# Performance work log

Measured on AMD Instinct MI355X. Metric: run time of the kernel, lower is better.

Reference implementation:

```python
import jax, jax.numpy as jnp
import numpy as np

N = 100000   # nodes
E = 1600000  # edges (avg degree 16)
D = 128      # embedding / hidden dim
L = 2        # aggregator layers (len(weight_size_list)-1)
EPS = 1e-12  # F.normalize eps


def setup_inputs() -> dict:
    key = jax.random.key(0)
    ks = jax.random.split(key, 8)
    return {
        "embeddings": jax.random.normal(ks[0], (N, D), jnp.float32),
        "edge_src": jax.random.randint(ks[1], (E,), 0, N, jnp.int32),
        "edge_dst": jax.random.randint(ks[2], (E,), 0, N, jnp.int32),
        "edge_val": jax.random.uniform(ks[3], (E,), jnp.float32),
        "W_sum": jax.random.normal(ks[4], (L, D, D), jnp.float32) * 0.05,
        "b_sum": jnp.zeros((L, D), jnp.float32),
        "W_prod": jax.random.normal(ks[5], (L, D, D), jnp.float32) * 0.05,
        "b_prod": jnp.zeros((L, D), jnp.float32),
    }


def reference(embeddings, edge_src, edge_dst, edge_val, W_sum, b_sum, W_prod, b_prod):
    # Faithful KGATConv forward with BiAggregator (alg_type='bi'), dropout=0 (eval).
    # Note: original code feeds the UN-normalized aggregator output as `embeddings`
    # (ego) to the next layer, while the SpMM consumes the normalized all_embeddings[-1].
    ego = embeddings            # `embeddings` variable in torch code
    spmm_in = embeddings        # all_embeddings[-1]
    outs = [embeddings]
    for i in range(L):
        # sparse A @ x : gather source rows, scale by edge value, scatter-add to dst
        msg = edge_val[:, None] * spmm_in[edge_src]            # [E, D]
        side = jax.ops.segment_sum(msg, edge_dst, num_segments=N)  # [N, D]
        # BiAggregator: LeakyReLU(W1(e+side)+b1) + LeakyReLU(W2(e*side)+b2)
        s = jax.nn.leaky_relu((ego + side) @ W_sum[i] + b_sum[i], 0.01)
        p = jax.nn.leaky_relu((ego * side) @ W_prod[i] + b_prod[i], 0.01)
        ego = s + p
        # F.normalize(p=2, dim=-1)
        nrm = jnp.maximum(jnp.linalg.norm(ego, axis=-1, keepdims=True), EPS)
        spmm_in = ego / nrm
        outs.append(spmm_in)
    return jnp.stack(outs)  # [L+1, N, D]
```

## Files before the change

kernel.cpp:

```cpp
#include <hip/hip_runtime.h>

#define D_DIM 128
#define ROWS 32
#define MROWS 64
#define ZPAD 136
#define EPAD 132

#define BSH 7
#define BROWS (1 << BSH)
#define NB_MAX 2048
#define CHUNK 4096

typedef __bf16 bf16x8 __attribute__((ext_vector_type(8)));
typedef __bf16 bf16x4 __attribute__((ext_vector_type(4)));
typedef float  f32x4  __attribute__((ext_vector_type(4)));

__global__ __launch_bounds__(256) void spmm_atomic(
    const float* __restrict__ x, const int* __restrict__ src,
    const int* __restrict__ dst, const float* __restrict__ val,
    float* __restrict__ side, long long total)
{
    long long i = (long long)blockIdx.x * blockDim.x + threadIdx.x;
    if (i >= total) return;
    int e = (int)(i >> 5);
    int q = (int)(i & 31);
    int s = src[e];
    int d = dst[e];
    float v = val[e];
    const float4 xv = *reinterpret_cast<const float4*>(x + (long long)s * D_DIM + q * 4);
    float* o = side + (long long)d * D_DIM + q * 4;
    unsafeAtomicAdd(o + 0, v * xv.x);
    unsafeAtomicAdd(o + 1, v * xv.y);
    unsafeAtomicAdd(o + 2, v * xv.z);
    unsafeAtomicAdd(o + 3, v * xv.w);
}

__global__ __launch_bounds__(256) void hist_kernel(
    const int* __restrict__ dst, int* __restrict__ cnt, int E)
{
    int i = blockIdx.x * 256 + threadIdx.x;
    if (i < E) atomicAdd(&cnt[dst[i]], 1);
}

__global__ __launch_bounds__(256) void scan_blocks(
    const int* __restrict__ cnt, int* __restrict__ row_ptr,
    int* __restrict__ blk_sums, int N)
{
    __shared__ int sh[256];
    int i = blockIdx.x * 256 + threadIdx.x;
    int v = (i < N) ? cnt[i] : 0;
    sh[threadIdx.x] = v;
    __syncthreads();
#pragma unroll
    for (int off = 1; off < 256; off <<= 1) {
        int t = (threadIdx.x >= off) ? sh[threadIdx.x - off] : 0;
        __syncthreads();
        sh[threadIdx.x] += t;
        __syncthreads();
    }
    if (i < N) row_ptr[i] = sh[threadIdx.x] - v;
    if (threadIdx.x == 255) blk_sums[blockIdx.x] = sh[255];
}

__global__ __launch_bounds__(256) void scan_carry(int* __restrict__ blk, int B)
{
    __shared__ int sh[256];
    __shared__ int carry;
    if (threadIdx.x == 0) carry = 0;
    __syncthreads();
    for (int base = 0; base < B; base += 256) {
        int i = base + threadIdx.x;
        int v = (i < B) ? blk[i] : 0;
        sh[threadIdx.x] = v;
        __syncthreads();
#pragma unroll
        for (int off = 1; off < 256; off <<= 1) {
            int t = (threadIdx.x >= off) ? sh[threadIdx.x - off] : 0;
            __syncthreads();
            sh[threadIdx.x] += t;
            __syncthreads();
        }
        int excl = sh[threadIdx.x] - v + carry;
        if (i < B) blk[i] = excl;
        __syncthreads();
        if (threadIdx.x == 255) carry = carry + sh[255];
        __syncthreads();
    }
}

__global__ __launch_bounds__(256) void scan_add(
    int* __restrict__ row_ptr, const int* __restrict__ blk_sums,
    int* __restrict__ row_fill, int N, int E)
{
    int i = blockIdx.x * 256 + threadIdx.x;
    if (i < N) {
        int v = row_ptr[i] + blk_sums[i >> 8];
        row_ptr[i]  = v;
        row_fill[i] = v;
    }
    if (i == 0) row_ptr[N] = E;
}

__global__ __launch_bounds__(256) void scatter_kernel(
    const int* __restrict__ src, const int* __restrict__ dst,
    const float* __restrict__ val, int* __restrict__ row_fill,
    int2* __restrict__ csr_sv, int E)
{
    int e = blockIdx.x * 256 + threadIdx.x;
    if (e >= E) return;
    int d = dst[e];
    int pos = atomicAdd(&row_fill[d], 1);
    csr_sv[pos] = make_int2(src[e], __float_as_int(val[e]));
}

__global__ __launch_bounds__(256) void bucket_count(
    const int* __restrict__ dst, int* __restrict__ bucket_cnt, int E, int NB)
{
    __shared__ int h[NB_MAX];
    for (int i = threadIdx.x; i < NB; i += 256) h[i] = 0;
    __syncthreads();
    int ebase = blockIdx.x * CHUNK;
    int ecnt  = min(CHUNK, E - ebase);
    for (int i = threadIdx.x; i < ecnt; i += 256)
        atomicAdd(&h[dst[ebase + i] >> BSH], 1);
    __syncthreads();
    for (int i = threadIdx.x; i < NB; i += 256)
        if (h[i]) atomicAdd(&bucket_cnt[i], h[i]);
}

__global__ __launch_bounds__(256) void bucket_scan(
    const int* __restrict__ bucket_cnt, int* __restrict__ bucket_ptr,
    int* __restrict__ bucket_fill, int NB, int E)
{
    __shared__ int sh[256];
    __shared__ int carry;
    if (threadIdx.x == 0) carry = 0;
    __syncthreads();
    for (int base = 0; base < NB; base += 256) {
        int i = base + threadIdx.x;
        int v = (i < NB) ? bucket_cnt[i] : 0;
        sh[threadIdx.x] = v;
        __syncthreads();
#pragma unroll
        for (int off = 1; off < 256; off <<= 1) {
            int t = (threadIdx.x >= off) ? sh[threadIdx.x - off] : 0;
            __syncthreads();
            sh[threadIdx.x] += t;
            __syncthreads();
        }
        if (i < NB) {
            int excl = sh[threadIdx.x] - v + carry;
            bucket_ptr[i]  = excl;
            bucket_fill[i] = excl;
        }
        __syncthreads();
        if (threadIdx.x == 255) carry = carry + sh[255];
        __syncthreads();
    }
    if (threadIdx.x == 0) bucket_ptr[NB] = E;
}

__global__ __launch_bounds__(256) void bucket_scatter(
    const int* __restrict__ src, const int* __restrict__ dst,
    const float* __restrict__ val, int* __restrict__ bucket_fill,
    int* __restrict__ stage,
    int NB, int E)
{
    __shared__ int hist[NB_MAX];
    __shared__ int excl[NB_MAX];
    __shared__ int gbase[NB_MAX];
    __shared__ int psum[256];
    __shared__ int s_src[CHUNK];
    __shared__ int s_val[CHUNK];
    __shared__ int s_dst[CHUNK];

    const int tid   = threadIdx.x;
    const int ebase = blockIdx.x * CHUNK;
    const int ecnt  = min(CHUNK, E - ebase);

    for (int i = tid; i < NB; i += 256) hist[i] = 0;
    __syncthreads();
    for (int i = tid; i < ecnt; i += 256)
        atomicAdd(&hist[dst[ebase + i] >> BSH], 1);
    __syncthreads();
    const int per = (NB + 255) / 256;
    const int t0  = tid * per;
    int tsum = 0;
    for (int k = 0; k < per; ++k) {
        int idx = t0 + k;
        tsum += (idx < NB) ? hist[idx] : 0;
    }
    psum[tid] = tsum;
    __syncthreads();
#pragma unroll
    for (int off = 1; off < 256; off <<= 1) {
        int t = (tid >= off) ? psum[tid - off] : 0;
        __syncthreads();
        psum[tid] += t;
        __syncthreads();
    }
    int run = psum[tid] - tsum;
    for (int k = 0; k < per; ++k) {
        int idx = t0 + k;
        if (idx < NB) { excl[idx] = run; run += hist[idx]; }
    }
    __syncthreads();
    for (int i = tid; i < NB; i += 256)
        gbase[i] = hist[i] ? atomicAdd(&bucket_fill[i], hist[i]) : 0;
    __syncthreads();
    for (int i = tid; i < NB; i += 256) hist[i] = excl[i];
    __syncthreads();
    for (int i = tid; i < ecnt; i += 256) {
        int d = dst[ebase + i];
        int slot = atomicAdd(&hist[d >> BSH], 1);
        s_src[slot] = src[ebase + i];
        s_val[slot] = __float_as_int(val[ebase + i]);
        s_dst[slot] = d;
    }
    __syncthreads();
    for (int i = tid; i < ecnt; i += 256) {
        int d   = s_dst[i];
        int bkt = d >> BSH;
        int gpos = gbase[bkt] + (i - excl[bkt]);
        *reinterpret_cast<int4*>(stage + 4 * (long long)gpos) =
            make_int4(s_src[i], s_val[i], d, 0);
    }
}

__global__ __launch_bounds__(256) void bucket_finalize(
    const int* __restrict__ stage, const int* __restrict__ bucket_ptr,
    int* __restrict__ row_ptr, int2* __restrict__ csr_sv, int N, int E)
{
    __shared__ int cnt[BROWS];
    __shared__ int rbase[BROWS];

    const int b   = blockIdx.x;
    const int tid = threadIdx.x;
    const int e0  = bucket_ptr[b];
    const int e1  = bucket_ptr[b + 1];
    const int r0  = b << BSH;
    const int nrows = min(BROWS, N - r0);

    if (tid < BROWS) cnt[tid] = 0;
    __syncthreads();
    for (int i = e0 + tid; i < e1; i += 256)
        atomicAdd(&cnt[stage[4 * (long long)i + 2] & (BROWS - 1)], 1);
    __syncthreads();
    if (tid < BROWS) rbase[tid] = cnt[tid];
    __syncthreads();
#pragma unroll
    for (int off = 1; off < BROWS; off <<= 1) {
        int t = 0;
        if (tid < BROWS && tid >= off) t = rbase[tid - off];
        __syncthreads();
        if (tid < BROWS) rbase[tid] += t;
        __syncthreads();
    }
    if (tid < BROWS) {
        int excl = e0 + rbase[tid] - cnt[tid];
        rbase[tid] = excl;
        if (tid < nrows) row_ptr[r0 + tid] = excl;
    }
    if (b == 0 && tid == 0) row_ptr[N] = E;
    __syncthreads();
    if (tid < BROWS) cnt[tid] = 0;
    __syncthreads();
    for (int i = e0 + tid; i < e1; i += 256) {
        const int4 t = *reinterpret_cast<const int4*>(stage + 4 * (long long)i);
        int r = t.z & (BROWS - 1);
        int rank = atomicAdd(&cnt[r], 1);
        csr_sv[rbase[r] + rank] = make_int2(t.x, t.y);
    }
}

__global__ __launch_bounds__(256) void wt_convert(
    const float* __restrict__ Wsum, const float* __restrict__ Wprod,
    __bf16* __restrict__ WTsum, __bf16* __restrict__ WTprod, int total)
{
    int i = blockIdx.x * 256 + threadIdx.x;
    if (i >= total) return;
    int l  = i >> 14;
    int nk = i & 16383;
    int n  = nk >> 7;
    int k  = nk & 127;
    int widx = (l << 14) + (k << 7) + n;
    WTsum[i]  = (__bf16)Wsum[widx];
    WTprod[i] = (__bf16)Wprod[widx];
}

__global__ __launch_bounds__(256) void emb_prep(
    const float* __restrict__ emb, float* __restrict__ out0,
    __bf16* __restrict__ xbf, long long n4)
{
    long long i = (long long)blockIdx.x * 256 + threadIdx.x;
    if (i >= n4) return;
    float4 v = reinterpret_cast<const float4*>(emb)[i];
    reinterpret_cast<float4*>(out0)[i] = v;
    bf16x4 b;
    b[0] = (__bf16)v.x; b[1] = (__bf16)v.y;
    b[2] = (__bf16)v.z; b[3] = (__bf16)v.w;
    reinterpret_cast<bf16x4*>(xbf)[i] = b;
}

__global__ __launch_bounds__(256) void spmm_csr_bf16(
    const __bf16* __restrict__ x, const int* __restrict__ row_ptr,
    const int2* __restrict__ csr_sv, float* __restrict__ side, int N)
{
    int row  = blockIdx.x * 8 + (threadIdx.x >> 5);
    int lane = threadIdx.x & 31;
    if (row >= N) return;
    int start = row_ptr[row];
    int end   = row_ptr[row + 1];
    const __bf16* xl = x + lane * 4;
    float4 acc = make_float4(0.f, 0.f, 0.f, 0.f);
    int j = start;
    for (; j + 8 <= end; j += 8) {
        int2 sv0 = csr_sv[j + 0], sv1 = csr_sv[j + 1];
        int2 sv2 = csr_sv[j + 2], sv3 = csr_sv[j + 3];
        int2 sv4 = csr_sv[j + 4], sv5 = csr_sv[j + 5];
        int2 sv6 = csr_sv[j + 6], sv7 = csr_sv[j + 7];
        bf16x4 b0 = *reinterpret_cast<const bf16x4*>(xl + (long long)sv0.x * D_DIM);
        bf16x4 b1 = *reinterpret_cast<const bf16x4*>(xl + (long long)sv1.x * D_DIM);
        bf16x4 b2 = *reinterpret_cast<const bf16x4*>(xl + (long long)sv2.x * D_DIM);
        bf16x4 b3 = *reinterpret_cast<const bf16x4*>(xl + (long long)sv3.x * D_DIM);
        bf16x4 b4 = *reinterpret_cast<const bf16x4*>(xl + (long long)sv4.x * D_DIM);
        bf16x4 b5 = *reinterpret_cast<const bf16x4*>(xl + (long long)sv5.x * D_DIM);
        bf16x4 b6 = *reinterpret_cast<const bf16x4*>(xl + (long long)sv6.x * D_DIM);
        bf16x4 b7 = *reinterpret_cast<const bf16x4*>(xl + (long long)sv7.x * D_DIM);
        float v0 = __int_as_float(sv0.y), v1 = __int_as_float(sv1.y);
        float v2 = __int_as_float(sv2.y), v3 = __int_as_float(sv3.y);
        float v4 = __int_as_float(sv4.y), v5 = __int_as_float(sv5.y);
        float v6 = __int_as_float(sv6.y), v7 = __int_as_float(sv7.y);
        acc.x += v0 * (float)b0[0] + v1 * (float)b1[0] + v2 * (float)b2[0] + v3 * (float)b3[0];
        acc.y += v0 * (float)b0[1] + v1 * (float)b1[1] + v2 * (float)b2[1] + v3 * (float)b3[1];
        acc.z += v0 * (float)b0[2] + v1 * (float)b1[2] + v2 * (float)b2[2] + v3 * (float)b3[2];
        acc.w += v0 * (float)b0[3] + v1 * (float)b1[3] + v2 * (float)b2[3] + v3 * (float)b3[3];
        acc.x += v4 * (float)b4[0] + v5 * (float)b5[0] + v6 * (float)b6[0] + v7 * (float)b7[0];
        acc.y += v4 * (float)b4[1] + v5 * (float)b5[1] + v6 * (float)b6[1] + v7 * (float)b7[1];
        acc.z += v4 * (float)b4[2] + v5 * (float)b5[2] + v6 * (float)b6[2] + v7 * (float)b7[2];
        acc.w += v4 * (float)b4[3] + v5 * (float)b5[3] + v6 * (float)b6[3] + v7 * (float)b7[3];
    }
    for (; j + 4 <= end; j += 4) {
        int2 sv0 = csr_sv[j + 0], sv1 = csr_sv[j + 1];
        int2 sv2 = csr_sv[j + 2], sv3 = csr_sv[j + 3];
        bf16x4 b0 = *reinterpret_cast<const bf16x4*>(xl + (long long)sv0.x * D_DIM);
        bf16x4 b1 = *reinterpret_cast<const bf16x4*>(xl + (long long)sv1.x * D_DIM);
        bf16x4 b2 = *reinterpret_cast<const bf16x4*>(xl + (long long)sv2.x * D_DIM);
        bf16x4 b3 = *reinterpret_cast<const bf16x4*>(xl + (long long)sv3.x * D_DIM);
        float v0 = __int_as_float(sv0.y), v1 = __int_as_float(sv1.y);
        float v2 = __int_as_float(sv2.y), v3 = __int_as_float(sv3.y);
        acc.x += v0 * (float)b0[0] + v1 * (float)b1[0] + v2 * (float)b2[0] + v3 * (float)b3[0];
        acc.y += v0 * (float)b0[1] + v1 * (float)b1[1] + v2 * (float)b2[1] + v3 * (float)b3[1];
        acc.z += v0 * (float)b0[2] + v1 * (float)b1[2] + v2 * (float)b2[2] + v3 * (float)b3[2];
        acc.w += v0 * (float)b0[3] + v1 * (float)b1[3] + v2 * (float)b2[3] + v3 * (float)b3[3];
    }
    for (; j < end; ++j) {
        int2 sv = csr_sv[j];
        float v = __int_as_float(sv.y);
        bf16x4 b = *reinterpret_cast<const bf16x4*>(xl + (long long)sv.x * D_DIM);
        acc.x += v * (float)b[0];
        acc.y += v * (float)b[1];
        acc.z += v * (float)b[2];
        acc.w += v * (float)b[3];
    }
    *reinterpret_cast<float4*>(side + (long long)row * D_DIM + lane * 4) = acc;
}

__global__ __launch_bounds__(256) void spmm_csr_f32(
    const float* __restrict__ x, const int* __restrict__ row_ptr,
    const int2* __restrict__ csr_sv, float* __restrict__ side, int N)
{
    int row  = blockIdx.x * 8 + (threadIdx.x >> 5);
    int lane = threadIdx.x & 31;
    if (row >= N) return;
    int start = row_ptr[row];
    int end   = row_ptr[row + 1];
    const float* xl = x + lane * 4;
    float4 acc = make_float4(0.f, 0.f, 0.f, 0.f);
    int j = start;
    for (; j + 4 <= end; j += 4) {
        int2 sv0 = csr_sv[j + 0], sv1 = csr_sv[j + 1];
        int2 sv2 = csr_sv[j + 2], sv3 = csr_sv[j + 3];
        const float4 x0 = *reinterpret_cast<const float4*>(xl + (long long)sv0.x * D_DIM);
        const float4 x1 = *reinterpret_cast<const float4*>(xl + (long long)sv1.x * D_DIM);
        const float4 x2 = *reinterpret_cast<const float4*>(xl + (long long)sv2.x * D_DIM);
        const float4 x3 = *reinterpret_cast<const float4*>(xl + (long long)sv3.x * D_DIM);
        float v0 = __int_as_float(sv0.y), v1 = __int_as_float(sv1.y);
        float v2 = __int_as_float(sv2.y), v3 = __int_as_float(sv3.y);
        acc.x += v0 * x0.x + v1 * x1.x + v2 * x2.x + v3 * x3.x;
        acc.y += v0 * x0.y + v1 * x1.y + v2 * x2.y + v3 * x3.y;
        acc.z += v0 * x0.z + v1 * x1.z + v2 * x2.z + v3 * x3.z;
        acc.w += v0 * x0.w + v1 * x1.w + v2 * x2.w + v3 * x3.w;
    }
    for (; j < end; ++j) {
        int2 sv = csr_sv[j];
        float v = __int_as_float(sv.y);
        const float4 xv = *reinterpret_cast<const float4*>(xl + (long long)sv.x * D_DIM);
        acc.x += v * xv.x;
        acc.y += v * xv.y;
        acc.z += v * xv.z;
        acc.w += v * xv.w;
    }
    *reinterpret_cast<float4*>(side + (long long)row * D_DIM + lane * 4) = acc;
}

__global__ __launch_bounds__(256) void fused_layer_mfma(
    const float* __restrict__ ego_src, const float* __restrict__ nrm_in,
    const float* __restrict__ side,
    const __bf16* __restrict__ WTsum, const float* __restrict__ bsum,
    const __bf16* __restrict__ WTprod, const float* __restrict__ bprod,
    float* __restrict__ norm_out,
    __bf16* __restrict__ nbf_out,
    float* __restrict__ nrm_out,
    int N)
{
    __shared__ __align__(16) char smem[MROWS * ZPAD * 2 * sizeof(__bf16)];
    __shared__ float invs[MROWS];
    auto zt = reinterpret_cast<__bf16(*)[ZPAD]>(smem);
    auto mt = reinterpret_cast<__bf16(*)[ZPAD]>(smem + MROWS * ZPAD * sizeof(__bf16));
    auto et = reinterpret_cast<float(*)[EPAD]>(smem);

    const int tid  = threadIdx.x;
    const int row0 = blockIdx.x * MROWS;

    for (int idx = tid; idx < MROWS * 32; idx += 256) {
        int r = idx >> 5, q = idx & 31;
        int row = row0 + r;
        float4 e4 = make_float4(0.f, 0.f, 0.f, 0.f);
        float4 s4 = make_float4(0.f, 0.f, 0.f, 0.f);
        if (row < N) {
            e4 = *reinterpret_cast<const float4*>(ego_src + (long long)row * D_DIM + q * 4);
            s4 = *reinterpret_cast<const float4*>(side    + (long long)row * D_DIM + q * 4);
            if (nrm_in) {
                float sc = nrm_in[row];
                e4.x *= sc; e4.y *= sc; e4.z *= sc; e4.w *= sc;
            }
        }
        bf16x4 z4, m4;
        z4[0] = (__bf16)(e4.x + s4.x); z4[1] = (__bf16)(e4.y + s4.y);
        z4[2] = (__bf16)(e4.z + s4.z); z4[3] = (__bf16)(e4.w + s4.w);
        m4[0] = (__bf16)(e4.x * s4.x); m4[1] = (__bf16)(e4.y * s4.y);
        m4[2] = (__bf16)(e4.z * s4.z); m4[3] = (__bf16)(e4.w * s4.w);
        *reinterpret_cast<bf16x4*>(&zt[r][q * 4]) = z4;
        *reinterpret_cast<bf16x4*>(&mt[r][q * 4]) = m4;
    }
    __syncthreads();

    const int wave = tid >> 6;
    const int lane = tid & 63;
    const int ln   = lane & 15;
    const int quad = lane >> 4;
    const int mloc = wave * 16;

    f32x4 acc_s[8], acc_p[8];
#pragma unroll
    for (int nt = 0; nt < 8; ++nt) {
        acc_s[nt] = (f32x4){0.f, 0.f, 0.f, 0.f};
        acc_p[nt] = (f32x4){0.f, 0.f, 0.f, 0.f};
    }

#pragma unroll
    for (int ks = 0; ks < 4; ++ks) {
        const int k0 = ks * 32 + quad * 8;
        bf16x8 az = *reinterpret_cast<const bf16x8*>(&zt[mloc + ln][k0]);
        bf16x8 am = *reinterpret_cast<const bf16x8*>(&mt[mloc + ln][k0]);
#pragma unroll
        for (int nt = 0; nt < 8; ++nt) {
            const long long wofs = (long long)(nt * 16 + ln) * D_DIM + k0;
            bf16x8 bs = *reinterpret_cast<const bf16x8*>(WTsum  + wofs);
            bf16x8 bp = *reinterpret_cast<const bf16x8*>(WTprod + wofs);
            acc_s[nt] = __builtin_amdgcn_mfma_f32_16x16x32_bf16(az, bs, acc_s[nt], 0, 0, 0);
            acc_p[nt] = __builtin_amdgcn_mfma_f32_16x16x32_bf16(am, bp, acc_p[nt], 0, 0, 0);
        }
    }

    float bsv[8], bpv[8];
#pragma unroll
    for (int nt = 0; nt < 8; ++nt) {
        bsv[nt] = bsum[nt * 16 + ln];
        bpv[nt] = bprod[nt * 16 + ln];
    }
    float part[4] = {0.f, 0.f, 0.f, 0.f};
#pragma unroll
    for (int nt = 0; nt < 8; ++nt) {
#pragma unroll
        for (int r = 0; r < 4; ++r) {
            float sv = acc_s[nt][r] + bsv[nt];
            sv = sv > 0.f ? sv : 0.01f * sv;
            float pv = acc_p[nt][r] + bpv[nt];
            pv = pv > 0.f ? pv : 0.01f * pv;
            float e = sv + pv;
            acc_s[nt][r] = e;
            part[r] += e * e;
        }
    }
#pragma unroll
    for (int off = 1; off < 16; off <<= 1) {
#pragma unroll
        for (int r = 0; r < 4; ++r)
            part[r] += __shfl_xor(part[r], off, 16);
    }

    __syncthreads();

#pragma unroll
    for (int r = 0; r < 4; ++r) {
        const int rl = mloc + quad * 4 + r;
        float nrmv = fmaxf(sqrtf(part[r]), 1e-12f);
        if (ln == 0) {
            invs[rl] = 1.0f / nrmv;
            int row = row0 + rl;
            if (nrm_out && row < N) nrm_out[row] = nrmv;
        }
#pragma unroll
        for (int nt = 0; nt < 8; ++nt)
            et[rl][nt * 16 + ln] = acc_s[nt][r];
    }
    __syncthreads();

    for (int idx = tid; idx < MROWS * 32; idx += 256) {
        int r = idx >> 5, q = idx & 31;
        int row = row0 + r;
        if (row >= N) continue;
        float inv = invs[r];
        float4 e4 = *reinterpret_cast<const float4*>(&et[r][q * 4]);
        float4 n4 = make_float4(e4.x * inv, e4.y * inv, e4.z * inv, e4.w * inv);
        *reinterpret_cast<float4*>(norm_out + (long long)row * D_DIM + q * 4) = n4;
        if (nbf_out) {
            bf16x4 b4;
            b4[0] = (__bf16)n4.x; b4[1] = (__bf16)n4.y;
            b4[2] = (__bf16)n4.z; b4[3] = (__bf16)n4.w;
            *reinterpret_cast<bf16x4*>(nbf_out + (long long)row * D_DIM + q * 4) = b4;
        }
    }
}

__global__ __launch_bounds__(256) void fused_layer_f32(
    const float* __restrict__ ego, const float* __restrict__ side,
    const float* __restrict__ Wsum, const float* __restrict__ bsum,
    const float* __restrict__ Wprod, const float* __restrict__ bprod,
    float* __restrict__ ego_out, float* __restrict__ norm_out, int N)
{
    __shared__ float zt[ROWS][D_DIM];
    __shared__ float mt[ROWS][D_DIM];
    __shared__ float wsh[32][D_DIM];
    __shared__ float wph[32][D_DIM];

    const int tid  = threadIdx.x;
    const int row0 = blockIdx.x * ROWS;
    const int cg   = tid & 31;
    const int rg   = tid >> 5;

    for (int idx = tid; idx < ROWS * 32; idx += 256) {
        int r = idx >> 5, q = idx & 31;
        int row = row0 + r;
        float4 e4 = make_float4(0.f, 0.f, 0.f, 0.f);
        float4 s4 = make_float4(0.f, 0.f, 0.f, 0.f);
        if (row < N) {
            e4 = *reinterpret_cast<const float4*>(ego  + (long long)row * D_DIM + q * 4);
            s4 = *reinterpret_cast<const float4*>(side + (long long)row * D_DIM + q * 4);
        }
        float4 z4 = make_float4(e4.x + s4.x, e4.y + s4.y, e4.z + s4.z, e4.w + s4.w);
        float4 m4 = make_float4(e4.x * s4.x, e4.y * s4.y, e4.z * s4.z, e4.w * s4.w);
        *reinterpret_cast<float4*>(&zt[r][q * 4]) = z4;
        *reinterpret_cast<float4*>(&mt[r][q * 4]) = m4;
    }

    float acc_s[4][4], acc_p[4][4];
#pragma unroll
    for (int a = 0; a < 4; ++a)
#pragma unroll
        for (int b = 0; b < 4; ++b) { acc_s[a][b] = 0.f; acc_p[a][b] = 0.f; }

    for (int kc = 0; kc < D_DIM; kc += 32) {
        __syncthreads();
        for (int idx = tid; idx < 32 * 32; idx += 256) {
            int kk = idx >> 5, q = idx & 31;
            *reinterpret_cast<float4*>(&wsh[kk][q * 4]) =
                *reinterpret_cast<const float4*>(Wsum + (long long)(kc + kk) * D_DIM + q * 4);
            *reinterpret_cast<float4*>(&wph[kk][q * 4]) =
                *reinterpret_cast<const float4*>(Wprod + (long long)(kc + kk) * D_DIM + q * 4);
        }
        __syncthreads();
#pragma unroll 8
        for (int kk = 0; kk < 32; ++kk) {
            float4 w_s = *reinterpret_cast<const float4*>(&wsh[kk][cg * 4]);
            float4 w_p = *reinterpret_cast<const float4*>(&wph[kk][cg * 4]);
#pragma unroll
            for (int rr = 0; rr < 4; ++rr) {
                float z = zt[rg * 4 + rr][kc + kk];
                float m = mt[rg * 4 + rr][kc + kk];
                acc_s[rr][0] += z * w_s.x; acc_s[rr][1] += z * w_s.y;
                acc_s[rr][2] += z * w_s.z; acc_s[rr][3] += z * w_s.w;
                acc_p[rr][0] += m * w_p.x; acc_p[rr][1] += m * w_p.y;
                acc_p[rr][2] += m * w_p.z; acc_p[rr][3] += m * w_p.w;
            }
        }
    }

    const float4 bs = *reinterpret_cast<const float4*>(bsum  + cg * 4);
    const float4 bp = *reinterpret_cast<const float4*>(bprod + cg * 4);
    float ev[4][4];
    float part[4];
#pragma unroll
    for (int rr = 0; rr < 4; ++rr) {
        float bsv[4] = {bs.x, bs.y, bs.z, bs.w};
        float bpv[4] = {bp.x, bp.y, bp.z, bp.w};
        float acc = 0.f;
#pragma unroll
        for (int cc = 0; cc < 4; ++cc) {
            float sv = acc_s[rr][cc] + bsv[cc];
            sv = sv > 0.f ? sv : 0.01f * sv;
            float pv = acc_p[rr][cc] + bpv[cc];
            pv = pv > 0.f ? pv : 0.01f * pv;
            float e = sv + pv;
            ev[rr][cc] = e;
            acc += e * e;
        }
        part[rr] = acc;
    }
#pragma unroll
    for (int off = 1; off < 32; off <<= 1) {
#pragma unroll
        for (int rr = 0; rr < 4; ++rr)
            part[rr] += __shfl_xor(part[rr], off, 32);
    }
#pragma unroll
    for (int rr = 0; rr < 4; ++rr) {
        int row = row0 + rg * 4 + rr;
        if (row >= N) continue;
        float inv = 1.0f / fmaxf(sqrtf(part[rr]), 1e-12f);
        float4 o  = make_float4(ev[rr][0] * inv, ev[rr][1] * inv,
                                ev[rr][2] * inv, ev[rr][3] * inv);
        *reinterpret_cast<float4*>(norm_out + (long long)row * D_DIM + cg * 4) = o;
        if (ego_out) {
            float4 g = make_float4(ev[rr][0], ev[rr][1], ev[rr][2], ev[rr][3]);
            *reinterpret_cast<float4*>(ego_out + (long long)row * D_DIM + cg * 4) = g;
        }
    }
}

extern "C" void kernel_launch(void* const* d_in, const int* in_sizes, int n_in,
                              void* d_out, int out_size, void* d_ws, size_t ws_size,
                              hipStream_t stream)
{
    const float* emb   = (const float*)d_in[0];
    const int*   esrc  = (const int*)  d_in[1];
    const int*   edst  = (const int*)  d_in[2];
    const float* evalv = (const float*)d_in[3];
    const float* Wsum  = (const float*)d_in[4];
    const float* bsum  = (const float*)d_in[5];
    const float* Wprod = (const float*)d_in[6];
    const float* bprod = (const float*)d_in[7];
    float* out = (float*)d_out;

    const int D = 128;
    const int N = in_sizes[0] / D;
    const int E = in_sizes[1];
    const int L = in_sizes[5] / D;
    const size_t ND = (size_t)N * D;
    const int B = (N + 255) / 256;
    const int NB = (N + BROWS - 1) >> BSH;

    char* ws = (char*)d_ws;
    float* side    = (float*)ws;                 ws += ND * sizeof(float);
    float* ego_buf = (float*)ws;                 ws += ND * sizeof(float);
    int*   row_ptr  = (int*)ws;                  ws += (size_t)(N + 1) * sizeof(int);
    int*   row_fill = (int*)ws;                  ws += (size_t)N * sizeof(int);
    int*   blk_sums = (int*)ws;                  ws += (size_t)B * sizeof(int);
    ws = (char*)(((uintptr_t)ws + 15) & ~(uintptr_t)15);
    int2*  csr_sv   = (int2*)ws;                 ws += (size_t)E * sizeof(int2);
    size_t csr_bytes = (size_t)(ws - (char*)d_ws);
    __bf16* WTsum  = (__bf16*)ws;                ws += (size_t)L * D * D * sizeof(__bf16);
    __bf16* WTprod = (__bf16*)ws;                ws += (size_t)L * D * D * sizeof(__bf16);
    __bf16* xbf    = (__bf16*)ws;                ws += ND * sizeof(__bf16);
    float*  nrm_buf = (float*)ws;                ws += (size_t)N * sizeof(float);
    size_t mfma_bytes = (size_t)(ws - (char*)d_ws);
    int* bucket_cnt  = (int*)ws;                 ws += (size_t)(NB + 1) * sizeof(int);
    int* bucket_ptr  = (int*)ws;                 ws += (size_t)(NB + 1) * sizeof(int);
    int* bucket_fill = (int*)ws;                 ws += (size_t)(NB + 1) * sizeof(int);
    size_t bucket_bytes = (size_t)(ws - (char*)d_ws);
    int* stage = (int*)side;

    const bool use_csr    = (ws_size >= csr_bytes);
    const bool use_mfma   = (ws_size >= mfma_bytes);
    const bool use_bucket = use_csr && (ws_size >= bucket_bytes) && (NB <= NB_MAX) &&
                            ((size_t)E * 16 <= 2 * ND * sizeof(float));

    if (use_mfma) {
        long long n4 = (long long)(ND / 4);
        emb_prep<<<(int)((n4 + 255) / 256), 256, 0, stream>>>(emb, out, xbf, n4);
        int total = L * D * D;
        wt_convert<<<(total + 255) / 256, 256, 0, stream>>>(
            Wsum, Wprod, WTsum, WTprod, total);
    } else {
        hipMemcpyAsync(out, emb, ND * sizeof(float), hipMemcpyDeviceToDevice, stream);
    }

    if (use_bucket) {
        const int nblk = (E + CHUNK - 1) / CHUNK;
        hipMemsetAsync(bucket_cnt, 0, (size_t)NB * sizeof(int), stream);
        bucket_count<<<nblk, 256, 0, stream>>>(edst, bucket_cnt, E, NB);
        bucket_scan<<<1, 256, 0, stream>>>(bucket_cnt, bucket_ptr, bucket_fill, NB, E);
        bucket_scatter<<<nblk, 256, 0, stream>>>(
            esrc, edst, evalv, bucket_fill, stage, NB, E);
        bucket_finalize<<<NB, 256, 0, stream>>>(
            stage, bucket_ptr, row_ptr, csr_sv, N, E);
    } else if (use_csr) {
        hipMemsetAsync(row_fill, 0, (size_t)N * sizeof(int), stream);
        hist_kernel<<<(E + 255) / 256, 256, 0, stream>>>(edst, row_fill, E);
        scan_blocks<<<B, 256, 0, stream>>>(row_fill, row_ptr, blk_sums, N);
        scan_carry<<<1, 256, 0, stream>>>(blk_sums, B);
        scan_add<<<B, 256, 0, stream>>>(row_ptr, blk_sums, row_fill, N, E);
        scatter_kernel<<<(E + 255) / 256, 256, 0, stream>>>(
            esrc, edst, evalv, row_fill, csr_sv, E);
    }

    const float* ego      = emb;
    const float* nrm_prev = nullptr;
    const float* spmm_in  = emb;
    for (int l = 0; l < L; ++l) {
        if (use_csr) {
            if (use_mfma) {
                spmm_csr_bf16<<<(N + 7) / 8, 256, 0, stream>>>(
                    xbf, row_ptr, csr_sv, side, N);
            } else {
                spmm_csr_f32<<<(N + 7) / 8, 256, 0, stream>>>(
                    spmm_in, row_ptr, csr_sv, side, N);
            }
        } else {
            hipMemsetAsync(side, 0, ND * sizeof(float), stream);
            long long total  = (long long)E * 32;
            long long blocks = (total + 255) / 256;
            spmm_atomic<<<(int)blocks, 256, 0, stream>>>(spmm_in, esrc, edst, evalv,
                                                         side, total);
        }

        float* norm_out = out + (size_t)(l + 1) * ND;
        if (use_mfma) {
            const bool more = (l + 1 < L);
            __bf16* nbf  = more ? xbf : nullptr;
            float*  nrmo = more ? nrm_buf : nullptr;
            fused_layer_mfma<<<(N + MROWS - 1) / MROWS, 256, 0, stream>>>(
                ego, nrm_prev, side,
                WTsum + (size_t)l * D * D, bsum + (size_t)l * D,
                WTprod + (size_t)l * D * D, bprod + (size_t)l * D,
                norm_out, nbf, nrmo, N);
            ego      = norm_out;
            nrm_prev = nrm_buf;
        } else {
            float* ego_out = (l + 1 < L) ? ego_buf : nullptr;
            fused_layer_f32<<<(N + ROWS - 1) / ROWS, 256, 0, stream>>>(
                ego, side,
                Wsum + (size_t)l * D * D, bsum + (size_t)l * D,
                Wprod + (size_t)l * D * D, bprod + (size_t)l * D,
                ego_out, norm_out, N);
            ego     = ego_buf;
            spmm_in = norm_out;
        }
    }
}
```

Measured before the change: 613.8 us.

## Repartition fused MFMA layer so each wave owns an output column slice with register-resident weights

The fused layer kernel now uses 512 threads (8 waves), and each wave computes a 16-column slice of the output for all 64 rows, instead of each of 4 waves computing 16 rows across all 128 columns. Each wave loads its weight fragments once into registers before the barrier, so the weight loads overlap the staging of z/m tiles and are no longer re-read from global memory in the inner loop. Row norms become per-wave partial sums in shared memory, reduced in the final store loop. This trades more shared-memory traffic and an extra reduction step for fewer global weight loads and more waves per block.

After: 535.0 us. 1.15x faster.

```diff
diff --git a/kernel.cpp b/kernel.cpp
--- a/kernel.cpp
+++ b/kernel.cpp
@@ -404,7 +404,7 @@
     *reinterpret_cast<float4*>(side + (long long)row * D_DIM + lane * 4) = acc;
 }
 
-__global__ __launch_bounds__(256) void fused_layer_mfma(
+__global__ __launch_bounds__(512) void fused_layer_mfma(
     const float* __restrict__ ego_src, const float* __restrict__ nrm_in,
     const float* __restrict__ side,
     const __bf16* __restrict__ WTsum, const float* __restrict__ bsum,
@@ -415,7 +415,7 @@
     int N)
 {
     __shared__ __align__(16) char smem[MROWS * ZPAD * 2 * sizeof(__bf16)];
-    __shared__ float invs[MROWS];
+    __shared__ float rowsq[MROWS][9];
     auto zt = reinterpret_cast<__bf16(*)[ZPAD]>(smem);
     auto mt = reinterpret_cast<__bf16(*)[ZPAD]>(smem + MROWS * ZPAD * sizeof(__bf16));
     auto et = reinterpret_cast<float(*)[EPAD]>(smem);
@@ -423,7 +423,7 @@
     const int tid  = threadIdx.x;
     const int row0 = blockIdx.x * MROWS;
 
-    for (int idx = tid; idx < MROWS * 32; idx += 256) {
+    for (int idx = tid; idx < MROWS * 32; idx += 512) {
         int r = idx >> 5, q = idx & 31;
         int row = row0 + r;
         float4 e4 = make_float4(0.f, 0.f, 0.f, 0.f);
@@ -444,85 +444,81 @@
         *reinterpret_cast<bf16x4*>(&zt[r][q * 4]) = z4;
         *reinterpret_cast<bf16x4*>(&mt[r][q * 4]) = m4;
     }
-    __syncthreads();
 
     const int wave = tid >> 6;
     const int lane = tid & 63;
     const int ln   = lane & 15;
     const int quad = lane >> 4;
-    const int mloc = wave * 16;
-
-    f32x4 acc_s[8], acc_p[8];
-#pragma unroll
-    for (int nt = 0; nt < 8; ++nt) {
-        acc_s[nt] = (f32x4){0.f, 0.f, 0.f, 0.f};
-        acc_p[nt] = (f32x4){0.f, 0.f, 0.f, 0.f};
-    }
-
+
+    bf16x8 bs[4], bp[4];
 #pragma unroll
     for (int ks = 0; ks < 4; ++ks) {
-        const int k0 = ks * 32 + quad * 8;
-        bf16x8 az = *reinterpret_cast<const bf16x8*>(&zt[mloc + ln][k0]);
-        bf16x8 am = *reinterpret_cast<const bf16x8*>(&mt[mloc + ln][k0]);
-#pragma unroll
-        for (int nt = 0; nt < 8; ++nt) {
-            const long long wofs = (long long)(nt * 16 + ln) * D_DIM + k0;
-            bf16x8 bs = *reinterpret_cast<const bf16x8*>(WTsum  + wofs);
-            bf16x8 bp = *reinterpret_cast<const bf16x8*>(WTprod + wofs);
-            acc_s[nt] = __builtin_amdgcn_mfma_f32_16x16x32_bf16(az, bs, acc_s[nt], 0, 0, 0);
-            acc_p[nt] = __builtin_amdgcn_mfma_f32_16x16x32_bf16(am, bp, acc_p[nt], 0, 0, 0);
-        }
-    }
-
-    float bsv[8], bpv[8];
-#pragma unroll
-    for (int nt = 0; nt < 8; ++nt) {
-        bsv[nt] = bsum[nt * 16 + ln];
-        bpv[nt] = bprod[nt * 16 + ln];
-    }
-    float part[4] = {0.f, 0.f, 0.f, 0.f};
-#pragma unroll
-    for (int nt = 0; nt < 8; ++nt) {
+        const long long wofs = (long long)(wave * 16 + ln) * D_DIM + ks * 32 + quad * 8;
+        bs[ks] = *reinterpret_cast<const bf16x8*>(WTsum  + wofs);
+        bp[ks] = *reinterpret_cast<const bf16x8*>(WTprod + wofs);
+    }
+
+    __syncthreads();
+
+    f32x4 acc_s[4], acc_p[4];
+#pragma unroll
+    for (int rg = 0; rg < 4; ++rg) {
+        acc_s[rg] = (f32x4){0.f, 0.f, 0.f, 0.f};
+        acc_p[rg] = (f32x4){0.f, 0.f, 0.f, 0.f};
+    }
+
+#pragma unroll
+    for (int rg = 0; rg < 4; ++rg) {
+#pragma unroll
+        for (int ks = 0; ks < 4; ++ks) {
+            const int k0 = ks * 32 + quad * 8;
+            bf16x8 az = *reinterpret_cast<const bf16x8*>(&zt[rg * 16 + ln][k0]);
+            bf16x8 am = *reinterpret_cast<const bf16x8*>(&mt[rg * 16 + ln][k0]);
+            acc_s[rg] = __builtin_amdgcn_mfma_f32_16x16x32_bf16(az, bs[ks], acc_s[rg], 0, 0, 0);
+            acc_p[rg] = __builtin_amdgcn_mfma_f32_16x16x32_bf16(am, bp[ks], acc_p[rg], 0, 0, 0);
+        }
+    }
+
+    const float bsv = bsum[wave * 16 + ln];
+    const float bpv = bprod[wave * 16 + ln];
+#pragma unroll
+    for (int rg = 0; rg < 4; ++rg) {
 #pragma unroll
         for (int r = 0; r < 4; ++r) {
-            float sv = acc_s[nt][r] + bsv[nt];
+            float sv = acc_s[rg][r] + bsv;
             sv = sv > 0.f ? sv : 0.01f * sv;
-            float pv = acc_p[nt][r] + bpv[nt];
+            float pv = acc_p[rg][r] + bpv;
             pv = pv > 0.f ? pv : 0.01f * pv;
             float e = sv + pv;
-            acc_s[nt][r] = e;
-            part[r] += e * e;
-        }
-    }
-#pragma unroll
-    for (int off = 1; off < 16; off <<= 1) {
+            acc_s[rg][r] = e;
+            float sq = e * e;
+#pragma unroll
+            for (int off = 1; off < 16; off <<= 1)
+                sq += __shfl_xor(sq, off, 16);
+            if (ln == 0)
+                rowsq[rg * 16 + quad * 4 + r][wave] = sq;
+        }
+    }
+
+    __syncthreads();
+
+#pragma unroll
+    for (int rg = 0; rg < 4; ++rg)
 #pragma unroll
         for (int r = 0; r < 4; ++r)
-            part[r] += __shfl_xor(part[r], off, 16);
-    }
-
-    __syncthreads();
-
-#pragma unroll
-    for (int r = 0; r < 4; ++r) {
-        const int rl = mloc + quad * 4 + r;
-        float nrmv = fmaxf(sqrtf(part[r]), 1e-12f);
-        if (ln == 0) {
-            invs[rl] = 1.0f / nrmv;
-            int row = row0 + rl;
-            if (nrm_out && row < N) nrm_out[row] = nrmv;
-        }
-#pragma unroll
-        for (int nt = 0; nt < 8; ++nt)
-            et[rl][nt * 16 + ln] = acc_s[nt][r];
-    }
-    __syncthreads();
-
-    for (int idx = tid; idx < MROWS * 32; idx += 256) {
+            et[rg * 16 + quad * 4 + r][wave * 16 + ln] = acc_s[rg][r];
+    __syncthreads();
+
+    for (int idx = tid; idx < MROWS * 32; idx += 512) {
         int r = idx >> 5, q = idx & 31;
         int row = row0 + r;
         if (row >= N) continue;
-        float inv = invs[r];
+        float s = 0.f;
+#pragma unroll
+        for (int j = 0; j < 8; ++j) s += rowsq[r][j];
+        float nrmv = fmaxf(sqrtf(s), 1e-12f);
+        float inv  = 1.0f / nrmv;
+        if (q == 0 && nrm_out) nrm_out[row] = nrmv;
         float4 e4 = *reinterpret_cast<const float4*>(&et[r][q * 4]);
         float4 n4 = make_float4(e4.x * inv, e4.y * inv, e4.z * inv, e4.w * inv);
         *reinterpret_cast<float4*>(norm_out + (long long)row * D_DIM + q * 4) = n4;
@@ -741,7 +737,7 @@
             const bool more = (l + 1 < L);
             __bf16* nbf  = more ? xbf : nullptr;
             float*  nrmo = more ? nrm_buf : nullptr;
-            fused_layer_mfma<<<(N + MROWS - 1) / MROWS, 256, 0, stream>>>(
+            fused_layer_mfma<<<(N + MROWS - 1) / MROWS, 512, 0, stream>>>(
                 ego, nrm_prev, side,
                 WTsum + (size_t)l * D * D, bsum + (size_t)l * D,
                 WTprod + (size_t)l * D * D, bprod + (size_t)l * D,
```
